# Kernel tuning notes

Measured on AMD Instinct MI355X. Metric: run time of the kernel, lower is better.

Reference implementation:

```python
import jax, jax.numpy as jnp
import numpy as np
import math

# Shapes: b, coarse nodes, fine cells per coarse cell grouped as (seq_out, seq_in)
B, N_OUT, SO, SI, NV, NC = 4, 10240, 4, 4, 1, 32
N_PHI, N_DIST, N_SIGMA = 4, 4, 1
DIST_UNIT = 2.0  # (global_level_no - global_level_encode) * grid_layer_encode.nh_dist
MIN_SIGMA = 1e-10


def setup_inputs() -> dict:
    key = jax.random.key(0)
    k1, k2, k3 = jax.random.split(key, 3)
    n_in = N_OUT * SO * SI
    # x: (b, n_in, nh_in=1, nv, nc), nh_in_encode=False path (x.unsqueeze(2))
    x = jax.random.normal(k1, (B, n_in, 1, NV, NC), dtype=jnp.float32)
    # relative coordinates (cartesian, rotated frame): (1, n_out, seq_out, seq_in)
    coords_x = jax.random.uniform(k2, (1, N_OUT, SO, SI), dtype=jnp.float32,
                                  minval=-DIST_UNIT, maxval=DIST_UNIT)
    coords_y = jax.random.uniform(k3, (1, N_OUT, SO, SI), dtype=jnp.float32,
                                  minval=-DIST_UNIT, maxval=DIST_UNIT)
    # parameters exactly as in __init__
    phis = jnp.linspace(-jnp.pi, jnp.pi, N_PHI + 1)[:-1].astype(jnp.float32)
    d = jnp.arange(1, 2 * N_DIST, 2, dtype=jnp.float32) / (N_DIST * 2)
    dists_param = -jnp.log(1.0 / d - 1.0)  # inverse-sigmoid init
    s = 1.0 / (2 * N_DIST * math.sqrt(2 * math.log(2)))
    sigma_param = (-math.log(1.0 / s - 1.0)) * jnp.ones((N_SIGMA,), jnp.float32)
    return dict(x=x, coords_x=coords_x, coords_y=coords_y,
                phis=phis, dists_param=dists_param, sigma_param=sigma_param)


def reference(x, coords_x, coords_y, phis, dists_param, sigma_param):
    b = x.shape[0]
    nv, nc = x.shape[-2], x.shape[-1]
    n_out, so, si = coords_x.shape[1], coords_x.shape[2], coords_x.shape[3]

    # get_spatial_weights
    dists = DIST_UNIT * jax.nn.sigmoid(dists_param)              # (D,)
    mu_x = jnp.cos(phis)[:, None] * dists[None, :]               # (P, D)
    mu_y = jnp.sin(phis)[:, None] * dists[None, :]               # (P, D)
    sigma = jnp.maximum(DIST_UNIT * jax.nn.sigmoid(sigma_param), MIN_SIGMA)  # (S,)

    dx = coords_x[0][..., None, None] - mu_x                     # (O, so, si, P, D)
    dy = coords_y[0][..., None, None] - mu_y                     # (O, so, si, P, D)
    w = jnp.exp(-0.5 * (dx * dx + dy * dy)[..., None] / (sigma * sigma))  # (O, so, si, P, D, S)

    # mult_weights_t (n_out <= n_in branch): normalize over the (so, si) receptive field
    w = w / (w.sum(axis=(1, 2), keepdims=True) + 1e-20)

    # grouped view: n_in = n_out * so * si, nh_in = 1
    xr = x.reshape(b, n_out, so, si, nv, nc)
    # weighted reduce over the receptive field against mixture weights
    out = jnp.einsum('boijvc,oijpds->bovpdsc', xr, w)            # (b, O, nv, P, D, S, nc)
    return out
```

## Files before the change

### kernel.cpp

```cpp
#include <hip/hip_runtime.h>
#include <math.h>

namespace {

constexpr int NOUT = 10240;
constexpr int OPB  = 4;
constexpr int NIJ  = 16;
constexpr int NPD  = 16;
constexpr int NC   = 32;
constexpr int NIN  = NOUT * NIJ;
constexpr int WPAD = 20;

typedef float vfloat4 __attribute__((ext_vector_type(4)));

__device__ __forceinline__ void fma4(float4& a, float s, const float4& v) {
    a.x = fmaf(s, v.x, a.x);
    a.y = fmaf(s, v.y, a.y);
    a.z = fmaf(s, v.z, a.z);
    a.w = fmaf(s, v.w, a.w);
}

__device__ __forceinline__ void nt_store4(float4* p, const float4& v) {
    vfloat4 nv = { v.x, v.y, v.z, v.w };
    __builtin_nontemporal_store(nv, reinterpret_cast<vfloat4*>(p));
}

__global__ __launch_bounds__(256) void polnorm_kernel(
    const float* __restrict__ x,
    const float* __restrict__ cx,
    const float* __restrict__ cy,
    const float* __restrict__ phis,
    const float* __restrict__ dists_p,
    const float* __restrict__ sigma_p,
    float* __restrict__ out)
{
    __shared__ __align__(16) float s_w[OPB][NPD][WPAD];
    __shared__ float s_inv[OPB][NPD];
    __shared__ __align__(16) float s_x[4][NIJ * NC];

    const int t = threadIdx.x;
    const int o_base = blockIdx.x * OPB;

    const int wid = t >> 6;
    const int l   = t & 63;
    const int c4  = l & 7;
    const int pda = l >> 3;

    const float4* xg = reinterpret_cast<const float4*>(
        x + ((size_t)wid * NIN + (size_t)o_base * NIJ) * NC);
    float4* og = reinterpret_cast<float4*>(
        out + ((size_t)wid * NOUT + o_base) * (size_t)(NPD * NC));

    float4 f0 = xg[l];
    float4 f1 = xg[64 + l];
    float4 g0 = xg[128 + l];
    float4 g1 = xg[128 + 64 + l];

    {
        const int pd = t >> 4;
        const int ij = t & 15;
        const int p = pd >> 2, d = pd & 3;

        const float dist = 2.0f / (1.0f + expf(-dists_p[d]));
        const float phi  = phis[p];
        const float mux  = cosf(phi) * dist;
        const float muy  = sinf(phi) * dist;
        float sg = 2.0f / (1.0f + expf(-sigma_p[0]));
        sg = fmaxf(sg, 1e-10f);
        const float coef = -0.5f / (sg * sg);

        #pragma unroll
        for (int k = 0; k < OPB; ++k) {
            const int o = o_base + k;
            const float dx = cx[o * NIJ + ij] - mux;
            const float dy = cy[o * NIJ + ij] - muy;
            const float w = expf(coef * (dx * dx + dy * dy));
            s_w[k][pd][ij] = w;
            float s = w;
            s += __shfl_xor(s, 1);
            s += __shfl_xor(s, 2);
            s += __shfl_xor(s, 4);
            s += __shfl_xor(s, 8);
            if (ij == 0) s_inv[k][pd] = 1.0f / (s + 1e-20f);
        }
    }
    __syncthreads();

    float4* xs = reinterpret_cast<float4*>(s_x[wid]);

    #pragma unroll
    for (int oi = 0; oi < OPB; ++oi) {
        xs[l] = f0;
        xs[64 + l] = f1;

        f0 = g0; f1 = g1;
        if (oi + 2 < OPB) {
            g0 = xg[(oi + 2) * 128 + l];
            g1 = xg[(oi + 2) * 128 + 64 + l];
        }

        float4 acc0 = make_float4(0.f, 0.f, 0.f, 0.f);
        float4 acc1 = make_float4(0.f, 0.f, 0.f, 0.f);

        #pragma unroll
        for (int kk = 0; kk < 4; ++kk) {
            const float4 wa = *reinterpret_cast<const float4*>(&s_w[oi][pda][kk * 4]);
            const float4 wb = *reinterpret_cast<const float4*>(&s_w[oi][pda + 8][kk * 4]);
            const float4 xv0 = xs[(kk * 4 + 0) * 8 + c4];
            const float4 xv1 = xs[(kk * 4 + 1) * 8 + c4];
            const float4 xv2 = xs[(kk * 4 + 2) * 8 + c4];
            const float4 xv3 = xs[(kk * 4 + 3) * 8 + c4];
            fma4(acc0, wa.x, xv0); fma4(acc1, wb.x, xv0);
            fma4(acc0, wa.y, xv1); fma4(acc1, wb.y, xv1);
            fma4(acc0, wa.z, xv2); fma4(acc1, wb.z, xv2);
            fma4(acc0, wa.w, xv3); fma4(acc1, wb.w, xv3);
        }

        const float ia = s_inv[oi][pda];
        const float ib = s_inv[oi][pda + 8];
        acc0.x *= ia; acc0.y *= ia; acc0.z *= ia; acc0.w *= ia;
        acc1.x *= ib; acc1.y *= ib; acc1.z *= ib; acc1.w *= ib;

        nt_store4(&og[oi * 128 + l], acc0);
        nt_store4(&og[oi * 128 + 64 + l], acc1);
    }
}

}

extern "C" void kernel_launch(void* const* d_in, const int* in_sizes, int n_in,
                              void* d_out, int out_size, void* d_ws, size_t ws_size,
                              hipStream_t stream) {
    const float* x  = (const float*)d_in[0];
    const float* cx = (const float*)d_in[1];
    const float* cy = (const float*)d_in[2];
    const float* ph = (const float*)d_in[3];
    const float* dp = (const float*)d_in[4];
    const float* sp = (const float*)d_in[5];
    float* out = (float*)d_out;

    dim3 grid(NOUT / OPB);
    dim3 block(256);
    hipLaunchKernelGGL(polnorm_kernel, grid, block, 0, stream,
                       x, cx, cy, ph, dp, sp, out);
}
```

Measured before the change: 31.74 us.

## Assign one output node per wave and drop block-wide barrier

Each wave now handles a single output node across all four batches, where before each wave handled one batch across four nodes. Because every wave computes its own 16x16 weight tile and normalisation, the __syncthreads and the shared inverse array go away. Weights are built from vectorised float4 coordinate loads, and the inverse sums are passed between lanes with shuffles. Weights and transcendental setup are now computed once per node and reused across the batch. Global x and output accesses now jump by batch stride between iterations, which may reduce locality.

```diff
diff --git a/kernel.cpp b/kernel.cpp
--- a/kernel.cpp
+++ b/kernel.cpp
@@ -4,7 +4,8 @@
 namespace {
 
 constexpr int NOUT = 10240;
-constexpr int OPB  = 4;
+constexpr int OW   = 4;
+constexpr int NB   = 4;
 constexpr int NIJ  = 16;
 constexpr int NPD  = 16;
 constexpr int NC   = 32;
@@ -34,34 +35,34 @@
     const float* __restrict__ sigma_p,
     float* __restrict__ out)
 {
-    __shared__ __align__(16) float s_w[OPB][NPD][WPAD];
-    __shared__ float s_inv[OPB][NPD];
-    __shared__ __align__(16) float s_x[4][NIJ * NC];
+    __shared__ __align__(16) float s_w[OW][NPD][WPAD];
+    __shared__ __align__(16) float s_x[OW][NIJ * NC];
 
-    const int t = threadIdx.x;
-    const int o_base = blockIdx.x * OPB;
-
+    const int t   = threadIdx.x;
     const int wid = t >> 6;
     const int l   = t & 63;
     const int c4  = l & 7;
     const int pda = l >> 3;
 
-    const float4* xg = reinterpret_cast<const float4*>(
-        x + ((size_t)wid * NIN + (size_t)o_base * NIJ) * NC);
-    float4* og = reinterpret_cast<float4*>(
-        out + ((size_t)wid * NOUT + o_base) * (size_t)(NPD * NC));
+    const int o = blockIdx.x * OW + wid;
+
+    const float4* xg = reinterpret_cast<const float4*>(x) + (size_t)o * (NIJ * NC / 4);
+    float4*       og = reinterpret_cast<float4*>(out)     + (size_t)o * (NPD * NC / 4);
+    const size_t xstride = (size_t)NIN * NC / 4;
+    const size_t ostride = (size_t)NOUT * NPD * NC / 4;
 
     float4 f0 = xg[l];
     float4 f1 = xg[64 + l];
-    float4 g0 = xg[128 + l];
-    float4 g1 = xg[128 + 64 + l];
+    float4 g0 = xg[xstride + l];
+    float4 g1 = xg[xstride + 64 + l];
 
+    float inv0, inv1;
     {
-        const int pd = t >> 4;
-        const int ij = t & 15;
-        const int p = pd >> 2, d = pd & 3;
+        const int pdf = l >> 2;
+        const int ijq = (l & 3) * 4;
+        const int p = pdf >> 2, dd = pdf & 3;
 
-        const float dist = 2.0f / (1.0f + expf(-dists_p[d]));
+        const float dist = 2.0f / (1.0f + expf(-dists_p[dd]));
         const float phi  = phis[p];
         const float mux  = cosf(phi) * dist;
         const float muy  = sinf(phi) * dist;
@@ -69,34 +70,37 @@
         sg = fmaxf(sg, 1e-10f);
         const float coef = -0.5f / (sg * sg);
 
-        #pragma unroll
-        for (int k = 0; k < OPB; ++k) {
-            const int o = o_base + k;
-            const float dx = cx[o * NIJ + ij] - mux;
-            const float dy = cy[o * NIJ + ij] - muy;
-            const float w = expf(coef * (dx * dx + dy * dy));
-            s_w[k][pd][ij] = w;
-            float s = w;
-            s += __shfl_xor(s, 1);
-            s += __shfl_xor(s, 2);
-            s += __shfl_xor(s, 4);
-            s += __shfl_xor(s, 8);
-            if (ij == 0) s_inv[k][pd] = 1.0f / (s + 1e-20f);
-        }
+        const float4 cxi = *reinterpret_cast<const float4*>(&cx[o * NIJ + ijq]);
+        const float4 cyi = *reinterpret_cast<const float4*>(&cy[o * NIJ + ijq]);
+
+        float4 w;
+        { float dx = cxi.x - mux, dy = cyi.x - muy; w.x = expf(coef * (dx*dx + dy*dy)); }
+        { float dx = cxi.y - mux, dy = cyi.y - muy; w.y = expf(coef * (dx*dx + dy*dy)); }
+        { float dx = cxi.z - mux, dy = cyi.z - muy; w.z = expf(coef * (dx*dx + dy*dy)); }
+        { float dx = cxi.w - mux, dy = cyi.w - muy; w.w = expf(coef * (dx*dx + dy*dy)); }
+
+        float s = w.x + w.y + w.z + w.w;
+        s += __shfl_xor(s, 1);
+        s += __shfl_xor(s, 2);
+        const float inv = 1.0f / (s + 1e-20f);
+
+        *reinterpret_cast<float4*>(&s_w[wid][pdf][ijq]) = w;
+
+        inv0 = __shfl(inv, pda * 4);
+        inv1 = __shfl(inv, pda * 4 + 32);
     }
-    __syncthreads();
 
     float4* xs = reinterpret_cast<float4*>(s_x[wid]);
 
     #pragma unroll
-    for (int oi = 0; oi < OPB; ++oi) {
+    for (int bi = 0; bi < NB; ++bi) {
         xs[l] = f0;
         xs[64 + l] = f1;
 
         f0 = g0; f1 = g1;
-        if (oi + 2 < OPB) {
-            g0 = xg[(oi + 2) * 128 + l];
-            g1 = xg[(oi + 2) * 128 + 64 + l];
+        if (bi + 2 < NB) {
+            g0 = xg[(size_t)(bi + 2) * xstride + l];
+            g1 = xg[(size_t)(bi + 2) * xstride + 64 + l];
         }
 
         float4 acc0 = make_float4(0.f, 0.f, 0.f, 0.f);
@@ -104,8 +108,8 @@
 
         #pragma unroll
         for (int kk = 0; kk < 4; ++kk) {
-            const float4 wa = *reinterpret_cast<const float4*>(&s_w[oi][pda][kk * 4]);
-            const float4 wb = *reinterpret_cast<const float4*>(&s_w[oi][pda + 8][kk * 4]);
+            const float4 wa = *reinterpret_cast<const float4*>(&s_w[wid][pda][kk * 4]);
+            const float4 wb = *reinterpret_cast<const float4*>(&s_w[wid][pda + 8][kk * 4]);
             const float4 xv0 = xs[(kk * 4 + 0) * 8 + c4];
             const float4 xv1 = xs[(kk * 4 + 1) * 8 + c4];
             const float4 xv2 = xs[(kk * 4 + 2) * 8 + c4];
@@ -116,13 +120,11 @@
             fma4(acc0, wa.w, xv3); fma4(acc1, wb.w, xv3);
         }
 
-        const float ia = s_inv[oi][pda];
-        const float ib = s_inv[oi][pda + 8];
-        acc0.x *= ia; acc0.y *= ia; acc0.z *= ia; acc0.w *= ia;
-        acc1.x *= ib; acc1.y *= ib; acc1.z *= ib; acc1.w *= ib;
+        acc0.x *= inv0; acc0.y *= inv0; acc0.z *= inv0; acc0.w *= inv0;
+        acc1.x *= inv1; acc1.y *= inv1; acc1.z *= inv1; acc1.w *= inv1;
 
-        nt_store4(&og[oi * 128 + l], acc0);
-        nt_store4(&og[oi * 128 + 64 + l], acc1);
+        nt_store4(&og[(size_t)bi * ostride + l], acc0);
+        nt_store4(&og[(size_t)bi * ostride + 64 + l], acc1);
     }
 }
 
@@ -139,7 +141,7 @@
     const float* sp = (const float*)d_in[5];
     float* out = (float*)d_out;
 
-    dim3 grid(NOUT / OPB);
+    dim3 grid(NOUT / OW);
     dim3 block(256);
     hipLaunchKernelGGL(polnorm_kernel, grid, block, 0, stream,
                        x, cx, cy, ph, dp, sp, out);
```

After: 33.37 us. 5.1% more time.
